# Kernel tuning notes

Hardware: AMD Instinct MI355X
Metric: run time of the kernel (lower is better)

The kernel has to match this reference:

```python
import jax, jax.numpy as jnp
import numpy as np

N_SRC_F = 40000; N_TGT_F = 40000; N_F = N_SRC_F + N_TGT_F
N_SRC_C = 1024; N_TGT_C = 1024; N_C = N_SRC_C + N_TGT_C
NN = 30        # KPConv neighbors per point
K = 15         # kernel points
C1 = 128       # fine-level feats (first_feats_dim)
C2 = 256       # coarse encoder out dim
GNN = 256      # gnn_feats_dim
HEADS = 4
DGCNN_K = 10
FINAL = 32     # final_feats_dim
EXT_F = 1.0; EXT_C = 2.0   # KPConv influence extents (scaled to unit-cube clouds)
EPS = 1e-12


def kpconv(q_pts, s_pts, s_feats, neighb, kpts, W, extent):
    # q_pts [Nq,3], s_pts [Ns,3], s_feats [Ns,Cin], neighb [Nq,NN], kpts [K,3], W [K,Cin,Cout]
    npts = s_pts[neighb]                              # [Nq,NN,3] irregular gather
    rel = npts - q_pts[:, None, :]
    # ||rel - kp||^2 expanded to avoid a [Nq,NN,K,3] intermediate
    d2 = (jnp.sum(rel * rel, -1)[:, :, None] + jnp.sum(kpts * kpts, -1)[None, None, :]
          - 2.0 * jnp.einsum('njd,kd->njk', rel, kpts))
    infl = jax.nn.relu(1.0 - jnp.sqrt(jnp.maximum(d2, EPS)) / extent)   # [Nq,NN,K]
    nf = s_feats[neighb]                              # [Nq,NN,Cin]
    h = jnp.einsum('njk,njc->nkc', infl, nf)          # kernel-point aggregation
    return jnp.einsum('nkc,kcd->nd', h, W)


def knn_idx(coords, k):
    sq = jnp.sum(coords * coords, -1)
    d2 = sq[:, None] + sq[None, :] - 2.0 * (coords @ coords.T)
    return jax.lax.top_k(-d2, k)[1]


def self_layer(coords, x, W, b):
    # DGCNN edge conv: knn on coords, edge = [x_i, x_j - x_i], 1x1 conv + relu, max over k
    idx = knn_idx(coords, DGCNN_K)
    neigh = x[idx]                                    # [N,k,C]
    ctr = jnp.broadcast_to(x[:, None, :], neigh.shape)
    edge = jnp.concatenate([ctr, neigh - ctr], -1)    # [N,k,2C]
    return jnp.max(jax.nn.relu(edge @ W + b), axis=1)


def cross_layer(x, y, Wq, Wk, Wv, Wm, bm):
    # multi-head cross attention x <- y, residual MLP on [x, message]
    N, C = x.shape
    dh = C // HEADS
    q = (x @ Wq).reshape(N, HEADS, dh)
    k = (y @ Wk).reshape(-1, HEADS, dh)
    v = (y @ Wv).reshape(-1, HEADS, dh)
    attn = jax.nn.softmax(jnp.einsum('nhd,mhd->hnm', q, k) / float(np.sqrt(dh)), axis=-1)
    msg = jnp.einsum('hnm,mhd->nhd', attn, v).reshape(N, C)
    return x + jnp.concatenate([x, msg], -1) @ Wm + bm


def l2norm(x):
    return x / jnp.maximum(jnp.linalg.norm(x, axis=1, keepdims=True), EPS)


def _forward(points_f, points_c, features, kernel_points_f, kernel_points_c,
             W_kp1, W_kp2, W_bottle, b_bottle, W_self1, b_self1,
             Wq, Wk, Wv, W_cross, b_cross, W_self2, b_self2,
             W_proj, b_proj, W_score, b_score, epsilon, W_dec, b_dec,
             neighbors_f, pool_idx, upsample_idx, len_src_c):
    # --- encoder: fine KPConv + strided KPConv to coarse ---
    x_f = kpconv(points_f, points_f, features, neighbors_f, kernel_points_f, W_kp1, EXT_F)  # [N_f,C1]
    skip = x_f
    x_c = kpconv(points_c, points_f, x_f, pool_idx, kernel_points_c, W_kp2, EXT_C)          # [N_c,C2]
    feats_c = x_c @ W_bottle + b_bottle                # bottleneck 1x1 conv -> [N_c,GNN]
    src, tgt = feats_c[:len_src_c], feats_c[len_src_c:]
    sc, tc = points_c[:len_src_c], points_c[len_src_c:]
    # --- GCN: self -> cross -> self (weights shared across src/tgt) ---
    src = self_layer(sc, src, W_self1, b_self1)
    tgt = self_layer(tc, tgt, W_self1, b_self1)
    src2 = cross_layer(src, tgt, Wq, Wk, Wv, W_cross, b_cross)
    tgt2 = cross_layer(tgt, src, Wq, Wk, Wv, W_cross, b_cross)
    src = self_layer(sc, src2, W_self2, b_self2)
    tgt = self_layer(tc, tgt2, W_self2, b_self2)
    feats = jnp.concatenate([src, tgt], 0) @ W_proj + b_proj   # proj_gnn
    scores_c_raw = feats @ W_score + b_score                   # proj_score [N_c,1]
    feats_norm = l2norm(feats)
    # --- bidirectional temperature-softmax matching head ---
    ip = feats_norm[:len_src_c] @ feats_norm[len_src_c:].T     # [Ns,Nt]
    temperature = jnp.exp(epsilon) + 0.03
    s1 = jax.nn.softmax(ip / temperature, axis=1) @ scores_c_raw[len_src_c:]
    s2 = jax.nn.softmax(ip.T / temperature, axis=1) @ scores_c_raw[:len_src_c]
    scores_saliency = jnp.concatenate([s1, s2], 0)
    # condition=True, add_cross_overlap=True branch
    x = jnp.concatenate([scores_c_raw, scores_saliency, feats], 1)    # [N_c, GNN+2]
    # --- decoder: nearest upsample + skip concat + unary conv ---
    x = jnp.concatenate([x[upsample_idx], skip], 1)            # [N_f, GNN+2+C1]
    x = x @ W_dec + b_dec                                      # [N_f, FINAL+2]
    feats_f = l2norm(x[:, :FINAL])
    so = jnp.clip(jax.nn.sigmoid(x[:, FINAL]), 0.0, 1.0)
    ss = jnp.clip(jax.nn.sigmoid(x[:, FINAL + 1]), 0.0, 1.0)
    so = jnp.where(jnp.isnan(so) | jnp.isinf(so), 0.0, so)     # regular_score
    ss = jnp.where(jnp.isnan(ss) | jnp.isinf(ss), 0.0, ss)
    return feats_f, so, ss


def _p(k, shape, fan):
    return jax.random.normal(k, shape, jnp.float32) / float(np.sqrt(fan))


def setup_inputs() -> dict:
    key = jax.random.key(0)
    ks = jax.random.split(key, 24)
    inp = {}
    inp['points_f'] = jax.random.uniform(ks[0], (N_F, 3), jnp.float32)
    inp['points_c'] = jax.random.uniform(ks[1], (N_C, 3), jnp.float32)
    inp['features'] = jnp.ones((N_F, 1), jnp.float32)
    inp['kernel_points_f'] = jax.random.normal(ks[2], (K, 3), jnp.float32) * 0.3
    inp['kernel_points_c'] = jax.random.normal(ks[3], (K, 3), jnp.float32) * 0.6
    inp['W_kp1'] = _p(ks[4], (K, 1, C1), K)
    inp['W_kp2'] = _p(ks[5], (K, C1, C2), K * C1)
    inp['W_bottle'] = _p(ks[6], (C2, GNN), C2); inp['b_bottle'] = jnp.zeros((GNN,), jnp.float32)
    inp['W_self1'] = _p(ks[7], (2 * GNN, GNN), 2 * GNN); inp['b_self1'] = jnp.zeros((GNN,), jnp.float32)
    inp['Wq'] = _p(ks[8], (GNN, GNN), GNN)
    inp['Wk'] = _p(ks[9], (GNN, GNN), GNN)
    inp['Wv'] = _p(ks[10], (GNN, GNN), GNN)
    inp['W_cross'] = _p(ks[11], (2 * GNN, GNN), 2 * GNN); inp['b_cross'] = jnp.zeros((GNN,), jnp.float32)
    inp['W_self2'] = _p(ks[12], (2 * GNN, GNN), 2 * GNN); inp['b_self2'] = jnp.zeros((GNN,), jnp.float32)
    inp['W_proj'] = _p(ks[13], (GNN, GNN), GNN); inp['b_proj'] = jnp.zeros((GNN,), jnp.float32)
    inp['W_score'] = _p(ks[14], (GNN, 1), GNN); inp['b_score'] = jnp.zeros((1,), jnp.float32)
    inp['epsilon'] = jnp.array(-5.0, jnp.float32)
    inp['W_dec'] = _p(ks[15], (GNN + 2 + C1, FINAL + 2), GNN + 2 + C1); inp['b_dec'] = jnp.zeros((FINAL + 2,), jnp.float32)
    inp['neighbors_f'] = jax.random.randint(ks[16], (N_F, NN), 0, N_F)
    inp['pool_idx'] = jax.random.randint(ks[17], (N_C, NN), 0, N_F)
    inp['upsample_idx'] = jax.random.randint(ks[18], (N_F,), 0, N_C)
    inp['len_src_c'] = N_SRC_C
    inp['len_src_f'] = N_SRC_F
    return inp


def reference(points_f, points_c, features, kernel_points_f, kernel_points_c,
              W_kp1, W_kp2, W_bottle, b_bottle, W_self1, b_self1,
              Wq, Wk, Wv, W_cross, b_cross, W_self2, b_self2,
              W_proj, b_proj, W_score, b_score, epsilon, W_dec, b_dec,
              neighbors_f, pool_idx, upsample_idx, len_src_c, len_src_f):
    return _forward(points_f, points_c, features, kernel_points_f, kernel_points_c,
                    W_kp1, W_kp2, W_bottle, b_bottle, W_self1, b_self1,
                    Wq, Wk, Wv, W_cross, b_cross, W_self2, b_self2,
                    W_proj, b_proj, W_score, b_score, epsilon, W_dec, b_dec,
                    neighbors_f, pool_idx, upsample_idx, len_src_c)
```

## Files before the change

### kernel.cpp

```cpp
#include <hip/hip_runtime.h>
#include <math.h>

#define NFINE   80000
#define NCRS    2048
#define NSRC    1024
#define NNB     30
#define KP      15
#define C1D     128
#define C2D     256
#define GD      256
#define DGK     10
#define FINALD  32
#define DECOUT  34

#define NCHUNK  8
#define CHUNK   128
#define TK      32
#define KC      4
#define KSTEP   480
#define GTR     16

__global__ __launch_bounds__(256) void kpconv_fine(
    const float* __restrict__ pts, const float* __restrict__ feat,
    const int* __restrict__ nbr, const float* __restrict__ kp,
    const float* __restrict__ W, float* __restrict__ out)
{
    int t = threadIdx.x, w = t >> 6, lane = t & 63;
    int n = blockIdx.x * 4 + w;
    __shared__ float contrib[4][NNB][17];
    __shared__ float h[4][KP + 1];
    float kx[KP], ky[KP], kz[KP], kk[KP];
#pragma unroll
    for (int k = 0; k < KP; k++) {
        kx[k] = kp[k*3]; ky[k] = kp[k*3+1]; kz[k] = kp[k*3+2];
        kk[k] = kx[k]*kx[k] + ky[k]*ky[k] + kz[k]*kz[k];
    }
    if (lane < NNB) {
        float qx = pts[n*3], qy = pts[n*3+1], qz = pts[n*3+2];
        int id = nbr[n*NNB + lane];
        float rx = pts[id*3]-qx, ry = pts[id*3+1]-qy, rz = pts[id*3+2]-qz;
        float rr = rx*rx + ry*ry + rz*rz;
        float f = feat[id];
#pragma unroll
        for (int k = 0; k < KP; k++) {
            float d2 = rr + kk[k] - 2.f*(rx*kx[k] + ry*ky[k] + rz*kz[k]);
            float infl = fmaxf(1.f - sqrtf(fmaxf(d2, 1e-12f)), 0.f);
            contrib[w][lane][k] = infl * f;
        }
    }
    __syncthreads();
// ... 65 lines not shown
    int t = threadIdx.x;
    int rg = blockIdx.x >> 2, kc = blockIdx.x & 3;
    int n0 = rg * GTR, kb0 = kc * KSTEP;
    __shared__ float xi[GTR][KSTEP];
    float* xf = &xi[0][0];
    for (int i = t; i < GTR*KSTEP; i += 256) {
        int r = i / KSTEP, c = i - r*KSTEP;
        xf[i] = hhg[(size_t)(n0 + r)*(KP*C1D) + kb0 + c];
    }
    __syncthreads();
    float a[GTR];
#pragma unroll
    for (int r = 0; r < GTR; r++) a[r] = 0.f;
    for (int c = 0; c < KSTEP; c += 4) {
        float w0 = W[(size_t)(kb0+c+0)*C2D + t];
        float w1 = W[(size_t)(kb0+c+1)*C2D + t];
        float w2 = W[(size_t)(kb0+c+2)*C2D + t];
        float w3 = W[(size_t)(kb0+c+3)*C2D + t];
#pragma unroll
        for (int r = 0; r < GTR; r++) {
            float4 xv = *(const float4*)&xi[r][c];
            a[r] += xv.x*w0 + xv.y*w1 + xv.z*w2 + xv.w*w3;
        }
    }
#pragma unroll
    for (int r = 0; r < GTR; r++)
        pbuf[(size_t)kc*NCRS*C2D + (size_t)(n0+r)*C2D + t] = a[r];
}

__global__ __launch_bounds__(256) void bottle_fused(
    const float* __restrict__ pbuf, const float* __restrict__ Wb,
    const float* __restrict__ b, float* __restrict__ out)
{
    int t = threadIdx.x, n0 = blockIdx.x * 8;
    const size_t MN = (size_t)NCRS*C2D;
    __shared__ float xi[8][C2D];
    for (int i = t; i < 8*C2D; i += 256) {
        int r = i >> 8, c = i & 255;
        size_t off = (size_t)(n0+r)*C2D + c;
        xi[r][c] = pbuf[off] + pbuf[MN+off] + pbuf[2*MN+off] + pbuf[3*MN+off];
    }
    __syncthreads();
    float a[8];
#pragma unroll
    for (int r = 0; r < 8; r++) a[r] = 0.f;
    for (int c = 0; c < C2D; c += 4) {
        float w0 = Wb[(c+0)*GD + t];
        float w1 = Wb[(c+1)*GD + t];
        float w2 = Wb[(c+2)*GD + t];
        float w3 = Wb[(c+3)*GD + t];
#pragma unroll
        for (int r = 0; r < 8; r++) {
            float4 xv = *(const float4*)&xi[r][c];
            a[r] += xv.x*w0 + xv.y*w1 + xv.z*w2 + xv.w*w3;
        }
    }
    float bv = b[t];
#pragma unroll
    for (int r = 0; r < 8; r++) out[(size_t)(n0+r)*GD + t] = a[r] + bv;
}

__global__ __launch_bounds__(512) void self_gemm(
    const float* __restrict__ x, const float* __restrict__ W,
    float* __restrict__ Y)
{
    int t = threadIdx.x, n0 = blockIdx.x * 8;
    __shared__ float xi[8][GD];
    for (int i = t; i < 8*GD; i += 512) {
        int r = i >> 8, c = i & 255;
        xi[r][c] = x[(size_t)(n0+r)*GD + c];
    }
    __syncthreads();
    const float* wcol = (t < GD) ? (W + t) : (W + (size_t)GD*GD + (t - GD));
    float a[8];
#pragma unroll
    for (int r = 0; r < 8; r++) a[r] = 0.f;
    for (int c = 0; c < GD; c += 4) {
        float w0 = wcol[(size_t)(c+0)*GD];
        float w1 = wcol[(size_t)(c+1)*GD];
        float w2 = wcol[(size_t)(c+2)*GD];
        float w3 = wcol[(size_t)(c+3)*GD];
#pragma unroll
        for (int r = 0; r < 8; r++) {
            float4 xv = *(const float4*)&xi[r][c];
            a[r] += xv.x*w0 + xv.y*w1 + xv.z*w2 + xv.w*w3;
        }
    }
#pragma unroll
    for (int r = 0; r < 8; r++) Y[(size_t)(n0+r)*512 + t] = a[r];
}

__global__ __launch_bounds__(256) void edge_max(
    const float* __restrict__ Y, const int* __restrict__ knn,
    const float* __restrict__ b, float* __restrict__ out)
{
    int n = blockIdx.x, t = threadIdx.x;
    int base = (n < NSRC) ? 0 : NSRC;
    __shared__ int ids[DGK];
    if (t < DGK) ids[t] = base + knn[n*DGK + t];
    __syncthreads();
    float a  = Y[(size_t)n*512 + t];
    float bn = Y[(size_t)n*512 + GD + t];
    float cst = a - bn + b[t];
    float acc = 0.f;
#pragma unroll
    for (int j = 0; j < DGK; j++) {
        float bj = Y[(size_t)ids[j]*512 + GD + t];
        acc = fmaxf(acc, fmaxf(cst + bj, 0.f));
    }
    out[(size_t)n*GD + t] = acc;
}

__global__ __launch_bounds__(256) void qkv_kernel(
    const float* __restrict__ x, const float* __restrict__ Wq,
    const float* __restrict__ Wk, const float* __restrict__ Wv,
    float* __restrict__ qb, float* __restrict__ kb, float* __restrict__ vb)
{
    int t = threadIdx.x, n0 = blockIdx.x * 8;
    __shared__ float xi[8][GD];
    for (int i = t; i < 8*GD; i += 256) {
        int r = i >> 8, c = i & 255;
        xi[r][c] = x[(size_t)(n0+r)*GD + c];
    }
    __syncthreads();
    const float* Ws[3] = {Wq, Wk, Wv};
    float* outs[3] = {qb, kb, vb};
#pragma unroll
    for (int m = 0; m < 3; m++) {
        const float* W = Ws[m];
        float a[8];
#pragma unroll
        for (int r = 0; r < 8; r++) a[r] = 0.f;
        for (int c = 0; c < GD; c += 4) {
            float w0 = W[(c+0)*GD + t];
            float w1 = W[(c+1)*GD + t];
            float w2 = W[(c+2)*GD + t];
            float w3 = W[(c+3)*GD + t];
#pragma unroll
            for (int r = 0; r < 8; r++) {
                float4 xv = *(const float4*)&xi[r][c];
                a[r] += xv.x*w0 + xv.y*w1 + xv.z*w2 + xv.w*w3;
            }
        }
        float* o = outs[m];
#pragma unroll
        for (int r = 0; r < 8; r++) o[(size_t)(n0+r)*GD + t] = a[r];
    }
}

__global__ __launch_bounds__(256) void knn_kernel(
    const float* __restrict__ pts, int* __restrict__ knn)
{
    int g = blockIdx.x;
    int t = threadIdx.x;
    int base = (g < NSRC) ? 0 : NSRC;
    int local = g - base;
    const float* P = pts + (size_t)base*3;
    __shared__ float d2s[NSRC];
    __shared__ float wval[4];
    __shared__ int   widx[4];
    float qx = P[local*3], qy = P[local*3+1], qz = P[local*3+2];
    float sqn = qx*qx + qy*qy + qz*qz;
#pragma unroll
    for (int ii = 0; ii < 4; ii++) {
        int m = t + ii*256;
        float px = P[m*3], py = P[m*3+1], pz = P[m*3+2];
        float sqm = px*px + py*py + pz*pz;
        d2s[m] = sqn + sqm - 2.f*(qx*px + qy*py + qz*pz);
    }
    __syncthreads();
    for (int r = 0; r < DGK; r++) {
        float bv = 3.4e38f; int bidx = NSRC;
#pragma unroll
        for (int ii = 0; ii < 4; ii++) {
            int m = t + ii*256;
            float v = d2s[m];
            if (v < bv) { bv = v; bidx = m; }
        }
#pragma unroll
// ... 19 lines not shown
}

__global__ __launch_bounds__(256) void attn_flash(
    const float* __restrict__ qb, const float* __restrict__ kb,
    const float* __restrict__ vb, float* __restrict__ pm,
    float* __restrict__ pl, float* __restrict__ pacc)
{
    int bidx = blockIdx.x;
    int h = bidx & 3, chunk = (bidx >> 2) & 7, rb = bidx >> 5;
    int t = threadIdx.x;
    int u = t >> 2, li = t & 3;
    int row0 = rb * 128 + u * 2;
    int kbase = (row0 < NSRC) ? NSRC : 0;

    __shared__ float4 kt[2][TK][16];
    __shared__ float4 vt[2][TK][16];

    const float4* kb4 = (const float4*)kb;
    const float4* vb4 = (const float4*)vb;
    size_t gbase = ((size_t)(kbase + chunk*CHUNK)) * 64 + h*16;

    float4 q0[4], q1[4];
    const float4* qa = (const float4*)(qb + (size_t)row0*GD + h*64 + li*16);
    const float4* qc = (const float4*)(qb + (size_t)(row0+1)*GD + h*64 + li*16);
#pragma unroll
    for (int i = 0; i < 4; i++) { q0[i] = qa[i]; q1[i] = qc[i]; }
    float4 a0[4], a1[4];
#pragma unroll
    for (int i = 0; i < 4; i++) {
        a0[i] = make_float4(0.f, 0.f, 0.f, 0.f);
        a1[i] = make_float4(0.f, 0.f, 0.f, 0.f);
    }
    float mr0 = -INFINITY, lr0 = 0.f, mr1 = -INFINITY, lr1 = 0.f;

    int f0 = t, f1 = t + 256;
    float4 rk0, rk1, rv0, rv1;

    {
        size_t tb = gbase;
        rk0 = kb4[tb + (size_t)(f0>>4)*64 + (f0&15)];
        rk1 = kb4[tb + (size_t)(f1>>4)*64 + (f1&15)];
        rv0 = vb4[tb + (size_t)(f0>>4)*64 + (f0&15)];
        rv1 = vb4[tb + (size_t)(f1>>4)*64 + (f1&15)];
        kt[0][f0>>4][f0&15] = rk0;  kt[0][f1>>4][f1&15] = rk1;
        vt[0][f0>>4][f0&15] = rv0;  vt[0][f1>>4][f1&15] = rv1;
    }
    __syncthreads();

    const int NT = CHUNK / TK;
    for (int tile = 0; tile < NT; tile++) {
        int cur = tile & 1;
        if (tile + 1 < NT) {
            size_t tb = gbase + (size_t)(tile+1)*TK*64;
            rk0 = kb4[tb + (size_t)(f0>>4)*64 + (f0&15)];
            rk1 = kb4[tb + (size_t)(f1>>4)*64 + (f1&15)];
            rv0 = vb4[tb + (size_t)(f0>>4)*64 + (f0&15)];
            rv1 = vb4[tb + (size_t)(f1>>4)*64 + (f1&15)];
        }
#pragma unroll 4
        for (int j = 0; j < TK; j++) {
            float4 k0 = kt[cur][j][li*4+0];
            float4 k1 = kt[cur][j][li*4+1];
            float4 k2 = kt[cur][j][li*4+2];
            float4 k3 = kt[cur][j][li*4+3];
            float pA = q0[0].x*k0.x + q0[0].y*k0.y + q0[0].z*k0.z + q0[0].w*k0.w
                     + q0[1].x*k1.x + q0[1].y*k1.y + q0[1].z*k1.z + q0[1].w*k1.w
                     + q0[2].x*k2.x + q0[2].y*k2.y + q0[2].z*k2.z + q0[2].w*k2.w
                     + q0[3].x*k3.x + q0[3].y*k3.y + q0[3].z*k3.z + q0[3].w*k3.w;
            float pB = q1[0].x*k0.x + q1[0].y*k0.y + q1[0].z*k0.z + q1[0].w*k0.w
                     + q1[1].x*k1.x + q1[1].y*k1.y + q1[1].z*k1.z + q1[1].w*k1.w
                     + q1[2].x*k2.x + q1[2].y*k2.y + q1[2].z*k2.z + q1[2].w*k2.w
                     + q1[3].x*k3.x + q1[3].y*k3.y + q1[3].z*k3.z + q1[3].w*k3.w;
            pA += __shfl_xor(pA, 1);  pB += __shfl_xor(pB, 1);
            pA += __shfl_xor(pA, 2);  pB += __shfl_xor(pB, 2);
            pA *= 0.125f;  pB *= 0.125f;
            float mn0 = fmaxf(mr0, pA);
            float mn1 = fmaxf(mr1, pB);
            float sc0 = __expf(mr0 - mn0), e0 = __expf(pA - mn0);
            float sc1 = __expf(mr1 - mn1), e1 = __expf(pB - mn1);
            lr0 = lr0*sc0 + e0;  lr1 = lr1*sc1 + e1;
            float4 v0 = vt[cur][j][li*4+0];
            float4 v1 = vt[cur][j][li*4+1];
            float4 v2 = vt[cur][j][li*4+2];
            float4 v3 = vt[cur][j][li*4+3];
            a0[0].x = a0[0].x*sc0 + e0*v0.x; a0[0].y = a0[0].y*sc0 + e0*v0.y;
            a0[0].z = a0[0].z*sc0 + e0*v0.z; a0[0].w = a0[0].w*sc0 + e0*v0.w;
            a0[1].x = a0[1].x*sc0 + e0*v1.x; a0[1].y = a0[1].y*sc0 + e0*v1.y;
            a0[1].z = a0[1].z*sc0 + e0*v1.z; a0[1].w = a0[1].w*sc0 + e0*v1.w;
            a0[2].x = a0[2].x*sc0 + e0*v2.x; a0[2].y = a0[2].y*sc0 + e0*v2.y;
            a0[2].z = a0[2].z*sc0 + e0*v2.z; a0[2].w = a0[2].w*sc0 + e0*v2.w;
            a0[3].x = a0[3].x*sc0 + e0*v3.x; a0[3].y = a0[3].y*sc0 + e0*v3.y;
            a0[3].z = a0[3].z*sc0 + e0*v3.z; a0[3].w = a0[3].w*sc0 + e0*v3.w;
            a1[0].x = a1[0].x*sc1 + e1*v0.x; a1[0].y = a1[0].y*sc1 + e1*v0.y;
            a1[0].z = a1[0].z*sc1 + e1*v0.z; a1[0].w = a1[0].w*sc1 + e1*v0.w;
            a1[1].x = a1[1].x*sc1 + e1*v1.x; a1[1].y = a1[1].y*sc1 + e1*v1.y;
            a1[1].z = a1[1].z*sc1 + e1*v1.z; a1[1].w = a1[1].w*sc1 + e1*v1.w;
            a1[2].x = a1[2].x*sc1 + e1*v2.x; a1[2].y = a1[2].y*sc1 + e1*v2.y;
            a1[2].z = a1[2].z*sc1 + e1*v2.z; a1[2].w = a1[2].w*sc1 + e1*v2.w;
            a1[3].x = a1[3].x*sc1 + e1*v3.x; a1[3].y = a1[3].y*sc1 + e1*v3.y;
            a1[3].z = a1[3].z*sc1 + e1*v3.z; a1[3].w = a1[3].w*sc1 + e1*v3.w;
            mr0 = mn0;  mr1 = mn1;
        }
        if (tile + 1 < NT) {
            __syncthreads();
            int nb = (tile + 1) & 1;
            kt[nb][f0>>4][f0&15] = rk0;  kt[nb][f1>>4][f1&15] = rk1;
            vt[nb][f0>>4][f0&15] = rv0;  vt[nb][f1>>4][f1&15] = rv1;
            __syncthreads();
        }
    }
    int pi0 = (chunk*4 + h)*NCRS + row0;
    if (li == 0) { pm[pi0] = mr0; pl[pi0] = lr0; pm[pi0+1] = mr1; pl[pi0+1] = lr1; }
    float4* po0 = (float4*)(pacc + (size_t)pi0*64);
    float4* po1 = (float4*)(pacc + (size_t)(pi0+1)*64);
#pragma unroll
    for (int i = 0; i < 4; i++) { po0[li*4 + i] = a0[i]; po1[li*4 + i] = a1[i]; }
}

__global__ __launch_bounds__(256) void attn_combine(
    const float* __restrict__ pm, const float* __restrict__ pl,
    const float* __restrict__ pacc, float* __restrict__ msg)
{
    int row = blockIdx.x, t = threadIdx.x;
    int h = t >> 6, d = t & 63;
    float m = -INFINITY;
#pragma unroll
    for (int c = 0; c < NCHUNK; c++) m = fmaxf(m, pm[(c*4 + h)*NCRS + row]);
    float lsum = 0.f, asum = 0.f;
#pragma unroll
    for (int c = 0; c < NCHUNK; c++) {
        int pi = (c*4 + h)*NCRS + row;
        float w = __expf(pm[pi] - m);
        lsum += pl[pi] * w;
        asum += pacc[(size_t)pi*64 + d] * w;
    }
    msg[(size_t)row*GD + h*64 + d] = asum / lsum;
}

__global__ __launch_bounds__(256) void cross_combine(
    const float* __restrict__ x, const float* __restrict__ msg,
    const float* __restrict__ Wm, const float* __restrict__ bm,
    float* __restrict__ out)
{
    int t = threadIdx.x, n0 = blockIdx.x * 8;
    __shared__ float xs[8][GD], ms[8][GD];
    for (int i = t; i < 8*GD; i += 256) {
        int r = i >> 8, c = i & 255;
        xs[r][c] = x[(size_t)(n0+r)*GD + c];
        ms[r][c] = msg[(size_t)(n0+r)*GD + c];
    }
    __syncthreads();
    float bv = bm[t];
    float a[8];
#pragma unroll
    for (int r = 0; r < 8; r++) a[r] = bv;
    for (int c = 0; c < GD; c += 4) {
        float w10 = Wm[(c+0)*GD + t];
        float w11 = Wm[(c+1)*GD + t];
        float w12 = Wm[(c+2)*GD + t];
        float w13 = Wm[(c+3)*GD + t];
        float w20 = Wm[(GD+c+0)*GD + t];
        float w21 = Wm[(GD+c+1)*GD + t];
        float w22 = Wm[(GD+c+2)*GD + t];
        float w23 = Wm[(GD+c+3)*GD + t];
#pragma unroll
        for (int r = 0; r < 8; r++) {
            float4 xv = *(const float4*)&xs[r][c];
            float4 mv = *(const float4*)&ms[r][c];
            a[r] += xv.x*w10 + xv.y*w11 + xv.z*w12 + xv.w*w13
                  + mv.x*w20 + mv.y*w21 + mv.z*w22 + mv.w*w23;
        }
    }
#pragma unroll
    for (int r = 0; r < 8; r++)
        out[(size_t)(n0+r)*GD + t] = xs[r][t] + a[r];
}

__global__ __launch_bounds__(256) void proj_gemm(
    const float* __restrict__ x, const float* __restrict__ W,
    const float* __restrict__ b, float* __restrict__ out)
{
    int t = threadIdx.x, n0 = blockIdx.x * 8;
    __shared__ float xi[8][GD];
    for (int i = t; i < 8*GD; i += 256) {
        int r = i >> 8, c = i & 255;
        xi[r][c] = x[(size_t)(n0+r)*GD + c];
    }
    __syncthreads();
    float a[8];
#pragma unroll
    for (int r = 0; r < 8; r++) a[r] = 0.f;
    for (int c = 0; c < GD; c += 4) {
        float w0 = W[(c+0)*GD + t];
        float w1 = W[(c+1)*GD + t];
        float w2 = W[(c+2)*GD + t];
        float w3 = W[(c+3)*GD + t];
#pragma unroll
        for (int r = 0; r < 8; r++) {
            float4 xv = *(const float4*)&xi[r][c];
            a[r] += xv.x*w0 + xv.y*w1 + xv.z*w2 + xv.w*w3;
        }
    }
    float bv = b[t];
#pragma unroll
    for (int r = 0; r < 8; r++) out[(size_t)(n0+r)*GD + t] = a[r] + bv;
}

__global__ __launch_bounds__(256) void norm_score(
    const float* __restrict__ feats, const float* __restrict__ Wsc,
    const float* __restrict__ bsc, float* __restrict__ fnorm,
    float* __restrict__ scores)
{
    int t = threadIdx.x, lane = t & 63, w = t >> 6;
    int n0 = blockIdx.x * 8;
#pragma unroll
    for (int rr = 0; rr < 2; rr++) {
        int r = n0 + w*2 + rr;
        float q0 = feats[(size_t)r*GD + lane];
        float q1 = feats[(size_t)r*GD + 64 + lane];
        float q2 = feats[(size_t)r*GD + 128 + lane];
        float q3 = feats[(size_t)r*GD + 192 + lane];
        float sq = q0*q0 + q1*q1 + q2*q2 + q3*q3;
        float sc = q0*Wsc[lane] + q1*Wsc[64+lane] + q2*Wsc[128+lane] + q3*Wsc[192+lane];
#pragma unroll
        for (int off = 32; off >= 1; off >>= 1) {
            sq += __shfl_xor(sq, off);
            sc += __shfl_xor(sc, off);
        }
        float inv = 1.f / fmaxf(sqrtf(sq), 1e-12f);
        fnorm[(size_t)r*GD + lane]       = q0*inv;
        fnorm[(size_t)r*GD + 64 + lane]  = q1*inv;
        fnorm[(size_t)r*GD + 128 + lane] = q2*inv;
        fnorm[(size_t)r*GD + 192 + lane] = q3*inv;
        if (lane == 0) scores[r] = sc + bsc[0];
    }
}

__global__ __launch_bounds__(256) void ip_kernel(
    const float* __restrict__ fnorm, float* __restrict__ ip)
{
    int t = threadIdx.x;
    int n0 = (blockIdx.x >> 2) * 4;
    int m  = (blockIdx.x & 3) * 256 + t;
    __shared__ float xs[GD][4];
    for (int i = t; i < 4*GD; i += 256) {
        int r = i >> 8, c = i & 255;
        xs[c][r] = fnorm[(size_t)(n0+r)*GD + c];
    }
    __syncthreads();
    const float4* fr = (const float4*)(fnorm + (size_t)(NSRC + m)*GD);
    float a0 = 0.f, a1 = 0.f, a2 = 0.f, a3 = 0.f;
    for (int c4 = 0; c4 < GD/4; c4++) {
        float4 f = fr[c4];
        float4 xa = *(const float4*)&xs[c4*4+0][0];
        float4 xb = *(const float4*)&xs[c4*4+1][0];
        float4 xc = *(const float4*)&xs[c4*4+2][0];
        float4 xd = *(const float4*)&xs[c4*4+3][0];
        a0 += f.x*xa.x + f.y*xb.x + f.z*xc.x + f.w*xd.x;
        a1 += f.x*xa.y + f.y*xb.y + f.z*xc.y + f.w*xd.y;
        a2 += f.x*xa.z + f.y*xb.z + f.z*xc.z + f.w*xd.z;
        a3 += f.x*xa.w + f.y*xb.w + f.z*xc.w + f.w*xd.w;
    }
    ip[(size_t)(n0+0)*NSRC + m] = a0;
    ip[(size_t)(n0+1)*NSRC + m] = a1;
    ip[(size_t)(n0+2)*NSRC + m] = a2;
    ip[(size_t)(n0+3)*NSRC + m] = a3;
}

template<bool COL>
__global__ __launch_bounds__(256) void saliency_kernel(
    const float* __restrict__ ip, const float* __restrict__ scores_other,
    const float* __restrict__ epsv, float* __restrict__ sal_out)
{
    int n = blockIdx.x, t = threadIdx.x;
    float T = expf(epsv[0]) + 0.03f;
    __shared__ float red[256];
    float vals[4];
    float m = -INFINITY;
#pragma unroll
    for (int ii = 0; ii < 4; ii++) {
        int i = t + ii*256;
        float vv = COL ? ip[(size_t)i*NSRC + n] : ip[(size_t)n*NSRC + i];
        vv /= T;
        vals[ii] = vv;
        m = fmaxf(m, vv);
    }
    red[t] = m; __syncthreads();
    for (int s = 128; s > 0; s >>= 1) { if (t < s) red[t] = fmaxf(red[t], red[t+s]); __syncthreads(); }
    float mx = red[0]; __syncthreads();
    float se = 0.f, wsum = 0.f;
#pragma unroll
    for (int ii = 0; ii < 4; ii++) {
        int i = t + ii*256;
        float e = expf(vals[ii] - mx);
        se += e; wsum += e * scores_other[i];
    }
    red[t] = se; __syncthreads();
    for (int s = 128; s > 0; s >>= 1) { if (t < s) red[t] += red[t+s]; __syncthreads(); }
    float S = red[0]; __syncthreads();
    red[t] = wsum; __syncthreads();
    for (int s = 128; s > 0; s >>= 1) { if (t < s) red[t] += red[t+s]; __syncthreads(); }
    if (t == 0) sal_out[n] = red[0] / S;
}

__global__ __launch_bounds__(256) void dec_coarse(
    const float* __restrict__ scores, const float* __restrict__ sal,
    const float* __restrict__ feats, const float* __restrict__ Wd,
    const float* __restrict__ bd, float* __restrict__ decfeat)
{
    int t = threadIdx.x, lane = t & 63, w = t >> 6;
    int n = blockIdx.x * 4 + w;
    __shared__ float xr[4][GD];
    for (int c = lane; c < GD; c += 64) xr[w][c] = feats[(size_t)n*GD + c];
    float acc = 0.f;
    if (lane < DECOUT) {
        acc = bd[lane] + scores[n]*Wd[lane] + sal[n]*Wd[DECOUT + lane];
        for (int c = 0; c < GD; c++) acc += xr[w][c] * Wd[(2 + c)*DECOUT + lane];
    }
    if (lane < 40) decfeat[(size_t)n*40 + lane] = (lane < DECOUT) ? acc : 0.f;
}

__global__ __launch_bounds__(256) void decoder_kernel(
    const float* __restrict__ decfeat, const float* __restrict__ skip,
    const int* __restrict__ ups, const float* __restrict__ Wd,
    float* __restrict__ outf, float* __restrict__ outso,
    float* __restrict__ outss)
{
    int t = threadIdx.x;
    __shared__ float wsk[C1D*36];
    for (int i = t; i < C1D*36; i += 256) {
        int cc = i / 36, j = i - cc*36;
        wsk[i] = (j < DECOUT) ? Wd[(size_t)(2 + GD + cc)*DECOUT + j] : 0.f;
    }
    __syncthreads();
    int row = blockIdx.x * 256 + t;
// ... 46 lines not shown
    const float* kp_c         = (const float*)d_in[4];
    const float* W_kp1        = (const float*)d_in[5];
    const float* W_kp2        = (const float*)d_in[6];
    const float* W_bottle     = (const float*)d_in[7];
    const float* b_bottle     = (const float*)d_in[8];
    const float* W_self1      = (const float*)d_in[9];
    const float* b_self1      = (const float*)d_in[10];
    const float* Wq           = (const float*)d_in[11];
    const float* Wk           = (const float*)d_in[12];
    const float* Wv           = (const float*)d_in[13];
    const float* W_cross      = (const float*)d_in[14];
    const float* b_cross      = (const float*)d_in[15];
    const float* W_self2      = (const float*)d_in[16];
    const float* b_self2      = (const float*)d_in[17];
    const float* W_proj       = (const float*)d_in[18];
    const float* b_proj       = (const float*)d_in[19];
    const float* W_score      = (const float*)d_in[20];
    const float* b_score      = (const float*)d_in[21];
    const float* epsilon      = (const float*)d_in[22];
    const float* W_dec        = (const float*)d_in[23];
    const float* b_dec        = (const float*)d_in[24];
    const int*   neighbors_f  = (const int*)d_in[25];
    const int*   pool_idx     = (const int*)d_in[26];
    const int*   upsample_idx = (const int*)d_in[27];

    float* ws = (float*)d_ws;
    size_t o = 0;
    auto alloc = [&](size_t nfl) { float* p = ws + o; o += (nfl + 63) & ~(size_t)63; return p; };
    float* x_f     = alloc((size_t)NFINE * C1D);
    float* g1      = alloc((size_t)NCRS * GD);
    float* qb      = alloc((size_t)NCRS * GD);
    float* kb      = alloc((size_t)NCRS * GD);
    float* vb      = alloc((size_t)NCRS * GD);
    float* msg     = alloc((size_t)NCRS * GD);
    float* feats_c = alloc((size_t)NCRS * GD);
    float* scores  = alloc(NCRS);
    float* sal     = alloc(NCRS);
    float* decfeat = alloc((size_t)NCRS * 40);
    int*   knn_b   = (int*)alloc(NCRS * DGK);

    const size_t NG = (size_t)NCRS * GD;
    const size_t MN = (size_t)NCRS * C2D;
    size_t usz = 4*MN + (size_t)NCRS*KP*C1D;
    float* U = alloc(usz);
    float* pbuf = U;
    float* hhg  = U + 4*MN;
    float* Y1   = U;
    float* pm   = U;
    float* pl   = U + (size_t)NCRS*4*NCHUNK;
    float* pacc = U + (size_t)2*NCRS*4*NCHUNK;
    float* g2   = U;
    float* Y2   = U + NG;
    float* g3   = U + 3*NG;
    float* feats= U + 4*NG;
    float* fnorm= U + 5*NG;
    float* ip   = U + 6*NG;

    float* outf  = (float*)d_out;
    float* outso = outf + (size_t)NFINE * FINALD;
    float* outss = outso + NFINE;

    kpconv_fine<<<NFINE/4, 256, 0, stream>>>(points_f, features, neighbors_f, kp_f, W_kp1, x_f);
    hh_kernel<<<NCRS, 256, 0, stream>>>(points_c, points_f, x_f, pool_idx, kp_c, hhg);
    hh_gemm<<<(NCRS/GTR)*KC, 256, 0, stream>>>(hhg, W_kp2, pbuf);
    bottle_fused<<<NCRS/8, 256, 0, stream>>>(pbuf, W_bottle, b_bottle, feats_c);

    knn_kernel<<<NCRS, 256, 0, stream>>>(points_c, knn_b);
    self_gemm<<<NCRS/8, 512, 0, stream>>>(feats_c, W_self1, Y1);
    edge_max<<<NCRS, 256, 0, stream>>>(Y1, knn_b, b_self1, g1);
    qkv_kernel<<<NCRS/8, 256, 0, stream>>>(g1, Wq, Wk, Wv, qb, kb, vb);
    attn_flash<<<512, 256, 0, stream>>>(qb, kb, vb, pm, pl, pacc);
    attn_combine<<<NCRS, 256, 0, stream>>>(pm, pl, pacc, msg);
    cross_combine<<<NCRS/8, 256, 0, stream>>>(g1, msg, W_cross, b_cross, g2);
    self_gemm<<<NCRS/8, 512, 0, stream>>>(g2, W_self2, Y2);
    edge_max<<<NCRS, 256, 0, stream>>>(Y2, knn_b, b_self2, g3);

    proj_gemm<<<NCRS/8, 256, 0, stream>>>(g3, W_proj, b_proj, feats);
    norm_score<<<NCRS/8, 256, 0, stream>>>(feats, W_score, b_score, fnorm, scores);
    ip_kernel<<<NSRC, 256, 0, stream>>>(fnorm, ip);
    saliency_kernel<false><<<NSRC, 256, 0, stream>>>(ip, scores + NSRC, epsilon, sal);
    saliency_kernel<true><<<NSRC, 256, 0, stream>>>(ip, scores, epsilon, sal + NSRC);

    dec_coarse<<<NCRS/4, 256, 0, stream>>>(scores, sal, feats, W_dec, b_dec, decfeat);
    decoder_kernel<<<(NFINE + 255)/256, 256, 0, stream>>>(decfeat, x_f, upsample_idx,
                                                          W_dec, outf, outso, outss);
}
```

Measured before the change: 499.9 us.

## Fuse attention combine, proj+norm, saliency kernels; halve GEMM row tiles; batch softmax

The attention combine step is folded into the cross-attention MLP kernel, and the projection GEMM is fused with L2-normalisation and scoring. The two saliency launches become one. Coarse GEMM kernels process 4 rows per block instead of 8, doubling block count for more parallelism on the 2048-row problems. The flash-attention inner loop now takes a per-tile max and rescales once per tile, with TK reduced to 16; this trades per-key rescale work for register arrays holding the scores.

```diff
diff --git a/kernel.cpp b/kernel.cpp
--- a/kernel.cpp
+++ b/kernel.cpp
@@ -15,7 +15,7 @@
 
 #define NCHUNK  8
 #define CHUNK   128
-#define TK      32
+#define TK      16
 #define KC      4
 #define KSTEP   480
 #define GTR     16
@@ -147,62 +147,62 @@
     const float* __restrict__ pbuf, const float* __restrict__ Wb,
     const float* __restrict__ b, float* __restrict__ out)
 {
-    int t = threadIdx.x, n0 = blockIdx.x * 8;
+    int t = threadIdx.x, n0 = blockIdx.x * 4;
     const size_t MN = (size_t)NCRS*C2D;
-    __shared__ float xi[8][C2D];
-    for (int i = t; i < 8*C2D; i += 256) {
+    __shared__ float xi[4][C2D];
+    for (int i = t; i < 4*C2D; i += 256) {
         int r = i >> 8, c = i & 255;
         size_t off = (size_t)(n0+r)*C2D + c;
         xi[r][c] = pbuf[off] + pbuf[MN+off] + pbuf[2*MN+off] + pbuf[3*MN+off];
     }
     __syncthreads();
-    float a[8];
-#pragma unroll
-    for (int r = 0; r < 8; r++) a[r] = 0.f;
+    float a[4];
+#pragma unroll
+    for (int r = 0; r < 4; r++) a[r] = 0.f;
     for (int c = 0; c < C2D; c += 4) {
         float w0 = Wb[(c+0)*GD + t];
         float w1 = Wb[(c+1)*GD + t];
         float w2 = Wb[(c+2)*GD + t];
         float w3 = Wb[(c+3)*GD + t];
 #pragma unroll
-        for (int r = 0; r < 8; r++) {
+        for (int r = 0; r < 4; r++) {
             float4 xv = *(const float4*)&xi[r][c];
             a[r] += xv.x*w0 + xv.y*w1 + xv.z*w2 + xv.w*w3;
         }
     }
     float bv = b[t];
 #pragma unroll
-    for (int r = 0; r < 8; r++) out[(size_t)(n0+r)*GD + t] = a[r] + bv;
+    for (int r = 0; r < 4; r++) out[(size_t)(n0+r)*GD + t] = a[r] + bv;
 }
 
 __global__ __launch_bounds__(512) void self_gemm(
     const float* __restrict__ x, const float* __restrict__ W,
     float* __restrict__ Y)
 {
-    int t = threadIdx.x, n0 = blockIdx.x * 8;
-    __shared__ float xi[8][GD];
-    for (int i = t; i < 8*GD; i += 512) {
+    int t = threadIdx.x, n0 = blockIdx.x * 4;
+    __shared__ float xi[4][GD];
+    for (int i = t; i < 4*GD; i += 512) {
         int r = i >> 8, c = i & 255;
         xi[r][c] = x[(size_t)(n0+r)*GD + c];
     }
     __syncthreads();
     const float* wcol = (t < GD) ? (W + t) : (W + (size_t)GD*GD + (t - GD));
-    float a[8];
-#pragma unroll
-    for (int r = 0; r < 8; r++) a[r] = 0.f;
+    float a[4];
+#pragma unroll
+    for (int r = 0; r < 4; r++) a[r] = 0.f;
     for (int c = 0; c < GD; c += 4) {
         float w0 = wcol[(size_t)(c+0)*GD];
         float w1 = wcol[(size_t)(c+1)*GD];
         float w2 = wcol[(size_t)(c+2)*GD];
         float w3 = wcol[(size_t)(c+3)*GD];
 #pragma unroll
-        for (int r = 0; r < 8; r++) {
+        for (int r = 0; r < 4; r++) {
             float4 xv = *(const float4*)&xi[r][c];
             a[r] += xv.x*w0 + xv.y*w1 + xv.z*w2 + xv.w*w3;
         }
     }
 #pragma unroll
-    for (int r = 0; r < 8; r++) Y[(size_t)(n0+r)*512 + t] = a[r];
+    for (int r = 0; r < 4; r++) Y[(size_t)(n0+r)*512 + t] = a[r];
 }
 
 __global__ __launch_bounds__(256) void edge_max(
@@ -231,9 +231,9 @@
     const float* __restrict__ Wk, const float* __restrict__ Wv,
     float* __restrict__ qb, float* __restrict__ kb, float* __restrict__ vb)
 {
-    int t = threadIdx.x, n0 = blockIdx.x * 8;
-    __shared__ float xi[8][GD];
-    for (int i = t; i < 8*GD; i += 256) {
+    int t = threadIdx.x, n0 = blockIdx.x * 4;
+    __shared__ float xi[4][GD];
+    for (int i = t; i < 4*GD; i += 256) {
         int r = i >> 8, c = i & 255;
         xi[r][c] = x[(size_t)(n0+r)*GD + c];
     }
@@ -243,23 +243,23 @@
 #pragma unroll
     for (int m = 0; m < 3; m++) {
         const float* W = Ws[m];
-        float a[8];
-#pragma unroll
-        for (int r = 0; r < 8; r++) a[r] = 0.f;
+        float a[4];
+#pragma unroll
+        for (int r = 0; r < 4; r++) a[r] = 0.f;
         for (int c = 0; c < GD; c += 4) {
             float w0 = W[(c+0)*GD + t];
             float w1 = W[(c+1)*GD + t];
             float w2 = W[(c+2)*GD + t];
             float w3 = W[(c+3)*GD + t];
 #pragma unroll
-            for (int r = 0; r < 8; r++) {
+            for (int r = 0; r < 4; r++) {
                 float4 xv = *(const float4*)&xi[r][c];
                 a[r] += xv.x*w0 + xv.y*w1 + xv.z*w2 + xv.w*w3;
             }
         }
         float* o = outs[m];
 #pragma unroll
-        for (int r = 0; r < 8; r++) o[(size_t)(n0+r)*GD + t] = a[r];
+        for (int r = 0; r < 4; r++) o[(size_t)(n0+r)*GD + t] = a[r];
     }
 }
 
@@ -345,18 +345,16 @@
         a1[i] = make_float4(0.f, 0.f, 0.f, 0.f);
     }
     float mr0 = -INFINITY, lr0 = 0.f, mr1 = -INFINITY, lr1 = 0.f;
-
-    int f0 = t, f1 = t + 256;
-    float4 rk0, rk1, rv0, rv1;
-
+    float p0[TK], p1[TK];
+
+    int f = t;
+    float4 rk, rv;
     {
         size_t tb = gbase;
-        rk0 = kb4[tb + (size_t)(f0>>4)*64 + (f0&15)];
-        rk1 = kb4[tb + (size_t)(f1>>4)*64 + (f1&15)];
-        rv0 = vb4[tb + (size_t)(f0>>4)*64 + (f0&15)];
-        rv1 = vb4[tb + (size_t)(f1>>4)*64 + (f1&15)];
-        kt[0][f0>>4][f0&15] = rk0;  kt[0][f1>>4][f1&15] = rk1;
-        vt[0][f0>>4][f0&15] = rv0;  vt[0][f1>>4][f1&15] = rv1;
+        rk = kb4[tb + (size_t)(f>>4)*64 + (f&15)];
+        rv = vb4[tb + (size_t)(f>>4)*64 + (f&15)];
+        kt[0][f>>4][f&15] = rk;
+        vt[0][f>>4][f&15] = rv;
     }
     __syncthreads();
 
@@ -365,12 +363,11 @@
         int cur = tile & 1;
         if (tile + 1 < NT) {
             size_t tb = gbase + (size_t)(tile+1)*TK*64;
-            rk0 = kb4[tb + (size_t)(f0>>4)*64 + (f0&15)];
-            rk1 = kb4[tb + (size_t)(f1>>4)*64 + (f1&15)];
-            rv0 = vb4[tb + (size_t)(f0>>4)*64 + (f0&15)];
-            rv1 = vb4[tb + (size_t)(f1>>4)*64 + (f1&15)];
-        }
-#pragma unroll 4
+            rk = kb4[tb + (size_t)(f>>4)*64 + (f&15)];
+            rv = vb4[tb + (size_t)(f>>4)*64 + (f&15)];
+        }
+        float tm0 = -INFINITY, tm1 = -INFINITY;
+#pragma unroll
         for (int j = 0; j < TK; j++) {
             float4 k0 = kt[cur][j][li*4+0];
             float4 k1 = kt[cur][j][li*4+1];
@@ -387,38 +384,41 @@
             pA += __shfl_xor(pA, 1);  pB += __shfl_xor(pB, 1);
             pA += __shfl_xor(pA, 2);  pB += __shfl_xor(pB, 2);
             pA *= 0.125f;  pB *= 0.125f;
-            float mn0 = fmaxf(mr0, pA);
-            float mn1 = fmaxf(mr1, pB);
-            float sc0 = __expf(mr0 - mn0), e0 = __expf(pA - mn0);
-            float sc1 = __expf(mr1 - mn1), e1 = __expf(pB - mn1);
-            lr0 = lr0*sc0 + e0;  lr1 = lr1*sc1 + e1;
+            p0[j] = pA;  p1[j] = pB;
+            tm0 = fmaxf(tm0, pA);  tm1 = fmaxf(tm1, pB);
+        }
+        float mn0 = fmaxf(mr0, tm0), mn1 = fmaxf(mr1, tm1);
+        float sc0 = __expf(mr0 - mn0), sc1 = __expf(mr1 - mn1);
+        lr0 *= sc0;  lr1 *= sc1;
+#pragma unroll
+        for (int i = 0; i < 4; i++) {
+            a0[i].x *= sc0; a0[i].y *= sc0; a0[i].z *= sc0; a0[i].w *= sc0;
+            a1[i].x *= sc1; a1[i].y *= sc1; a1[i].z *= sc1; a1[i].w *= sc1;
+        }
+        mr0 = mn0;  mr1 = mn1;
+#pragma unroll
+        for (int j = 0; j < TK; j++) {
+            float e0 = __expf(p0[j] - mn0);
+            float e1 = __expf(p1[j] - mn1);
+            lr0 += e0;  lr1 += e1;
             float4 v0 = vt[cur][j][li*4+0];
             float4 v1 = vt[cur][j][li*4+1];
             float4 v2 = vt[cur][j][li*4+2];
             float4 v3 = vt[cur][j][li*4+3];
-            a0[0].x = a0[0].x*sc0 + e0*v0.x; a0[0].y = a0[0].y*sc0 + e0*v0.y;
-            a0[0].z = a0[0].z*sc0 + e0*v0.z; a0[0].w = a0[0].w*sc0 + e0*v0.w;
-            a0[1].x = a0[1].x*sc0 + e0*v1.x; a0[1].y = a0[1].y*sc0 + e0*v1.y;
-            a0[1].z = a0[1].z*sc0 + e0*v1.z; a0[1].w = a0[1].w*sc0 + e0*v1.w;
-            a0[2].x = a0[2].x*sc0 + e0*v2.x; a0[2].y = a0[2].y*sc0 + e0*v2.y;
-            a0[2].z = a0[2].z*sc0 + e0*v2.z; a0[2].w = a0[2].w*sc0 + e0*v2.w;
-            a0[3].x = a0[3].x*sc0 + e0*v3.x; a0[3].y = a0[3].y*sc0 + e0*v3.y;
-            a0[3].z = a0[3].z*sc0 + e0*v3.z; a0[3].w = a0[3].w*sc0 + e0*v3.w;
-            a1[0].x = a1[0].x*sc1 + e1*v0.x; a1[0].y = a1[0].y*sc1 + e1*v0.y;
-            a1[0].z = a1[0].z*sc1 + e1*v0.z; a1[0].w = a1[0].w*sc1 + e1*v0.w;
-            a1[1].x = a1[1].x*sc1 + e1*v1.x; a1[1].y = a1[1].y*sc1 + e1*v1.y;
-            a1[1].z = a1[1].z*sc1 + e1*v1.z; a1[1].w = a1[1].w*sc1 + e1*v1.w;
-            a1[2].x = a1[2].x*sc1 + e1*v2.x; a1[2].y = a1[2].y*sc1 + e1*v2.y;
-            a1[2].z = a1[2].z*sc1 + e1*v2.z; a1[2].w = a1[2].w*sc1 + e1*v2.w;
-            a1[3].x = a1[3].x*sc1 + e1*v3.x; a1[3].y = a1[3].y*sc1 + e1*v3.y;
-            a1[3].z = a1[3].z*sc1 + e1*v3.z; a1[3].w = a1[3].w*sc1 + e1*v3.w;
-            mr0 = mn0;  mr1 = mn1;
+            a0[0].x += e0*v0.x; a0[0].y += e0*v0.y; a0[0].z += e0*v0.z; a0[0].w += e0*v0.w;
+            a0[1].x += e0*v1.x; a0[1].y += e0*v1.y; a0[1].z += e0*v1.z; a0[1].w += e0*v1.w;
+            a0[2].x += e0*v2.x; a0[2].y += e0*v2.y; a0[2].z += e0*v2.z; a0[2].w += e0*v2.w;
+            a0[3].x += e0*v3.x; a0[3].y += e0*v3.y; a0[3].z += e0*v3.z; a0[3].w += e0*v3.w;
+            a1[0].x += e1*v0.x; a1[0].y += e1*v0.y; a1[0].z += e1*v0.z; a1[0].w += e1*v0.w;
+            a1[1].x += e1*v1.x; a1[1].y += e1*v1.y; a1[1].z += e1*v1.z; a1[1].w += e1*v1.w;
+            a1[2].x += e1*v2.x; a1[2].y += e1*v2.y; a1[2].z += e1*v2.z; a1[2].w += e1*v2.w;
+            a1[3].x += e1*v3.x; a1[3].y += e1*v3.y; a1[3].z += e1*v3.z; a1[3].w += e1*v3.w;
         }
         if (tile + 1 < NT) {
             __syncthreads();
             int nb = (tile + 1) & 1;
-            kt[nb][f0>>4][f0&15] = rk0;  kt[nb][f1>>4][f1&15] = rk1;
-            vt[nb][f0>>4][f0&15] = rv0;  vt[nb][f1>>4][f1&15] = rv1;
+            kt[nb][f>>4][f&15] = rk;
+            vt[nb][f>>4][f&15] = rv;
             __syncthreads();
         }
     }
@@ -430,43 +430,38 @@
     for (int i = 0; i < 4; i++) { po0[li*4 + i] = a0[i]; po1[li*4 + i] = a1[i]; }
 }
 
-__global__ __launch_bounds__(256) void attn_combine(
-    const float* __restrict__ pm, const float* __restrict__ pl,
-    const float* __restrict__ pacc, float* __restrict__ msg)
-{
-    int row = blockIdx.x, t = threadIdx.x;
-    int h = t >> 6, d = t & 63;
-    float m = -INFINITY;
-#pragma unroll
-    for (int c = 0; c < NCHUNK; c++) m = fmaxf(m, pm[(c*4 + h)*NCRS + row]);
-    float lsum = 0.f, asum = 0.f;
-#pragma unroll
-    for (int c = 0; c < NCHUNK; c++) {
-        int pi = (c*4 + h)*NCRS + row;
-        float w = __expf(pm[pi] - m);
-        lsum += pl[pi] * w;
-        asum += pacc[(size_t)pi*64 + d] * w;
-    }
-    msg[(size_t)row*GD + h*64 + d] = asum / lsum;
-}
-
-__global__ __launch_bounds__(256) void cross_combine(
-    const float* __restrict__ x, const float* __restrict__ msg,
+__global__ __launch_bounds__(256) void cross_fused(
+    const float* __restrict__ x, const float* __restrict__ pm,
+    const float* __restrict__ pl, const float* __restrict__ pacc,
     const float* __restrict__ Wm, const float* __restrict__ bm,
     float* __restrict__ out)
 {
-    int t = threadIdx.x, n0 = blockIdx.x * 8;
-    __shared__ float xs[8][GD], ms[8][GD];
-    for (int i = t; i < 8*GD; i += 256) {
+    int t = threadIdx.x, n0 = blockIdx.x * 4;
+    int h = t >> 6, d = t & 63;
+    __shared__ float xs[4][GD], ms[4][GD];
+    for (int i = t; i < 4*GD; i += 256) {
         int r = i >> 8, c = i & 255;
         xs[r][c] = x[(size_t)(n0+r)*GD + c];
-        ms[r][c] = msg[(size_t)(n0+r)*GD + c];
+    }
+#pragma unroll
+    for (int r = 0; r < 4; r++) {
+        int row = n0 + r;
+        float m = -INFINITY;
+#pragma unroll
+        for (int c = 0; c < NCHUNK; c++) m = fmaxf(m, pm[(c*4 + h)*NCRS + row]);
+        float lsum = 0.f, asum = 0.f;
+#pragma unroll
+        for (int c = 0; c < NCHUNK; c++) {
+            int pi = (c*4 + h)*NCRS + row;
+            float w = __expf(pm[pi] - m);
+            lsum += pl[pi] * w;
+            asum += pacc[(size_t)pi*64 + d] * w;
+        }
+        ms[r][t] = asum / lsum;
     }
     __syncthreads();
     float bv = bm[t];
-    float a[8];
-#pragma unroll
-    for (int r = 0; r < 8; r++) a[r] = bv;
+    float a[4] = {bv, bv, bv, bv};
     for (int c = 0; c < GD; c += 4) {
         float w10 = Wm[(c+0)*GD + t];
         float w11 = Wm[(c+1)*GD + t];
@@ -477,7 +472,7 @@
         float w22 = Wm[(GD+c+2)*GD + t];
         float w23 = Wm[(GD+c+3)*GD + t];
 #pragma unroll
-        for (int r = 0; r < 8; r++) {
+        for (int r = 0; r < 4; r++) {
             float4 xv = *(const float4*)&xs[r][c];
             float4 mv = *(const float4*)&ms[r][c];
             a[r] += xv.x*w10 + xv.y*w11 + xv.z*w12 + xv.w*w13
@@ -485,68 +480,60 @@
         }
     }
 #pragma unroll
-    for (int r = 0; r < 8; r++)
+    for (int r = 0; r < 4; r++)
         out[(size_t)(n0+r)*GD + t] = xs[r][t] + a[r];
 }
 
-__global__ __launch_bounds__(256) void proj_gemm(
+__global__ __launch_bounds__(256) void proj_norm(
     const float* __restrict__ x, const float* __restrict__ W,
-    const float* __restrict__ b, float* __restrict__ out)
-{
-    int t = threadIdx.x, n0 = blockIdx.x * 8;
-    __shared__ float xi[8][GD];
-    for (int i = t; i < 8*GD; i += 256) {
+    const float* __restrict__ b, const float* __restrict__ Wsc,
+    const float* __restrict__ bsc, float* __restrict__ feats,
+    float* __restrict__ fnorm, float* __restrict__ scores)
+{
+    int t = threadIdx.x, n0 = blockIdx.x * 4;
+    __shared__ float xi[4][GD];
+    __shared__ float pf[4][GD];
+    for (int i = t; i < 4*GD; i += 256) {
         int r = i >> 8, c = i & 255;
         xi[r][c] = x[(size_t)(n0+r)*GD + c];
     }
     __syncthreads();
-    float a[8];
-#pragma unroll
-    for (int r = 0; r < 8; r++) a[r] = 0.f;
+    float a[4] = {0.f, 0.f, 0.f, 0.f};
     for (int c = 0; c < GD; c += 4) {
         float w0 = W[(c+0)*GD + t];
         float w1 = W[(c+1)*GD + t];
         float w2 = W[(c+2)*GD + t];
         float w3 = W[(c+3)*GD + t];
 #pragma unroll
-        for (int r = 0; r < 8; r++) {
+        for (int r = 0; r < 4; r++) {
             float4 xv = *(const float4*)&xi[r][c];
             a[r] += xv.x*w0 + xv.y*w1 + xv.z*w2 + xv.w*w3;
         }
     }
     float bv = b[t];
 #pragma unroll
-    for (int r = 0; r < 8; r++) out[(size_t)(n0+r)*GD + t] = a[r] + bv;
-}
-
-__global__ __launch_bounds__(256) void norm_score(
-    const float* __restrict__ feats, const float* __restrict__ Wsc,
-    const float* __restrict__ bsc, float* __restrict__ fnorm,
-    float* __restrict__ scores)
-{
-    int t = threadIdx.x, lane = t & 63, w = t >> 6;
-    int n0 = blockIdx.x * 8;
-#pragma unroll
-    for (int rr = 0; rr < 2; rr++) {
-        int r = n0 + w*2 + rr;
-        float q0 = feats[(size_t)r*GD + lane];
-        float q1 = feats[(size_t)r*GD + 64 + lane];
-        float q2 = feats[(size_t)r*GD + 128 + lane];
-        float q3 = feats[(size_t)r*GD + 192 + lane];
-        float sq = q0*q0 + q1*q1 + q2*q2 + q3*q3;
-        float sc = q0*Wsc[lane] + q1*Wsc[64+lane] + q2*Wsc[128+lane] + q3*Wsc[192+lane];
-#pragma unroll
-        for (int off = 32; off >= 1; off >>= 1) {
-            sq += __shfl_xor(sq, off);
-            sc += __shfl_xor(sc, off);
-        }
-        float inv = 1.f / fmaxf(sqrtf(sq), 1e-12f);
-        fnorm[(size_t)r*GD + lane]       = q0*inv;
-        fnorm[(size_t)r*GD + 64 + lane]  = q1*inv;
-        fnorm[(size_t)r*GD + 128 + lane] = q2*inv;
-        fnorm[(size_t)r*GD + 192 + lane] = q3*inv;
-        if (lane == 0) scores[r] = sc + bsc[0];
-    }
+    for (int r = 0; r < 4; r++) {
+        float v = a[r] + bv;
+        feats[(size_t)(n0+r)*GD + t] = v;
+        pf[r][t] = v;
+    }
+    __syncthreads();
+    int lane = t & 63, w = t >> 6;
+    int rr = n0 + w;
+    float q0 = pf[w][lane], q1 = pf[w][64+lane], q2 = pf[w][128+lane], q3 = pf[w][192+lane];
+    float sq = q0*q0 + q1*q1 + q2*q2 + q3*q3;
+    float sc = q0*Wsc[lane] + q1*Wsc[64+lane] + q2*Wsc[128+lane] + q3*Wsc[192+lane];
+#pragma unroll
+    for (int off = 32; off >= 1; off >>= 1) {
+        sq += __shfl_xor(sq, off);
+        sc += __shfl_xor(sc, off);
+    }
+    float inv = 1.f / fmaxf(sqrtf(sq), 1e-12f);
+    fnorm[(size_t)rr*GD + lane]       = q0*inv;
+    fnorm[(size_t)rr*GD + 64 + lane]  = q1*inv;
+    fnorm[(size_t)rr*GD + 128 + lane] = q2*inv;
+    fnorm[(size_t)rr*GD + 192 + lane] = q3*inv;
+    if (lane == 0) scores[rr] = sc + bsc[0];
 }
 
 __global__ __launch_bounds__(256) void ip_kernel(
@@ -580,12 +567,14 @@
     ip[(size_t)(n0+3)*NSRC + m] = a3;
 }
 
-template<bool COL>
-__global__ __launch_bounds__(256) void saliency_kernel(
-    const float* __restrict__ ip, const float* __restrict__ scores_other,
+__global__ __launch_bounds__(256) void saliency_all(
+    const float* __restrict__ ip, const float* __restrict__ scores,
     const float* __restrict__ epsv, float* __restrict__ sal_out)
 {
-    int n = blockIdx.x, t = threadIdx.x;
+    int g = blockIdx.x, t = threadIdx.x;
+    bool col = (g >= NSRC);
+    int n = col ? (g - NSRC) : g;
+    const float* so = col ? scores : (scores + NSRC);
     float T = expf(epsv[0]) + 0.03f;
     __shared__ float red[256];
     float vals[4];
@@ -593,7 +582,7 @@
 #pragma unroll
     for (int ii = 0; ii < 4; ii++) {
         int i = t + ii*256;
-        float vv = COL ? ip[(size_t)i*NSRC + n] : ip[(size_t)n*NSRC + i];
+        float vv = col ? ip[(size_t)i*NSRC + n] : ip[(size_t)n*NSRC + i];
         vv /= T;
         vals[ii] = vv;
         m = fmaxf(m, vv);
@@ -606,14 +595,14 @@
     for (int ii = 0; ii < 4; ii++) {
         int i = t + ii*256;
         float e = expf(vals[ii] - mx);
-        se += e; wsum += e * scores_other[i];
+        se += e; wsum += e * so[i];
     }
     red[t] = se; __syncthreads();
     for (int s = 128; s > 0; s >>= 1) { if (t < s) red[t] += red[t+s]; __syncthreads(); }
     float S = red[0]; __syncthreads();
     red[t] = wsum; __syncthreads();
     for (int s = 128; s > 0; s >>= 1) { if (t < s) red[t] += red[t+s]; __syncthreads(); }
-    if (t == 0) sal_out[n] = red[0] / S;
+    if (t == 0) sal_out[g] = red[0] / S;
 }
 
 __global__ __launch_bounds__(256) void dec_coarse(
@@ -726,7 +715,6 @@
     float* qb      = alloc((size_t)NCRS * GD);
     float* kb      = alloc((size_t)NCRS * GD);
     float* vb      = alloc((size_t)NCRS * GD);
-    float* msg     = alloc((size_t)NCRS * GD);
     float* feats_c = alloc((size_t)NCRS * GD);
     float* scores  = alloc(NCRS);
     float* sal     = alloc(NCRS);
@@ -735,21 +723,22 @@
 
     const size_t NG = (size_t)NCRS * GD;
     const size_t MN = (size_t)NCRS * C2D;
+    const size_t PMN = (size_t)NCRS * 4 * NCHUNK;
     size_t usz = 4*MN + (size_t)NCRS*KP*C1D;
     float* U = alloc(usz);
     float* pbuf = U;
     float* hhg  = U + 4*MN;
     float* Y1   = U;
     float* pm   = U;
-    float* pl   = U + (size_t)NCRS*4*NCHUNK;
-    float* pacc = U + (size_t)2*NCRS*4*NCHUNK;
-    float* g2   = U;
-    float* Y2   = U + NG;
-    float* g3   = U + 3*NG;
-    float* feats= U + 4*NG;
-    float* fnorm= U + 5*NG;
-    float* ip   = U + 6*NG;
-
+    float* pl   = U + PMN;
+    float* pacc = U + 2*PMN;
+    float* g2   = U + 2*PMN + PMN*64;
+    float* Y2   = U;
+    float* g3   = U + 2*NG;
+    float* feats= U + 3*NG;
+    float* fnorm= U + 4*NG;
+    float* ip   = U + 5*NG;
+    
     float* outf  = (float*)d_out;
     float* outso = outf + (size_t)NFINE * FINALD;
     float* outss = outso + NFINE;
@@ -757,23 +746,21 @@
     kpconv_fine<<<NFINE/4, 256, 0, stream>>>(points_f, features, neighbors_f, kp_f, W_kp1, x_f);
     hh_kernel<<<NCRS, 256, 0, stream>>>(points_c, points_f, x_f, pool_idx, kp_c, hhg);
     hh_gemm<<<(NCRS/GTR)*KC, 256, 0, stream>>>(hhg, W_kp2, pbuf);
-    bottle_fused<<<NCRS/8, 256, 0, stream>>>(pbuf, W_bottle, b_bottle, feats_c);
+    bottle_fused<<<NCRS/4, 256, 0, stream>>>(pbuf, W_bottle, b_bottle, feats_c);
 
     knn_kernel<<<NCRS, 256, 0, stream>>>(points_c, knn_b);
-    self_gemm<<<NCRS/8, 512, 0, stream>>>(feats_c, W_self1, Y1);
+    self_gemm<<<NCRS/4, 512, 0, stream>>>(feats_c, W_self1, Y1);
     edge_max<<<NCRS, 256, 0, stream>>>(Y1, knn_b, b_self1, g1);
-    qkv_kernel<<<NCRS/8, 256, 0, stream>>>(g1, Wq, Wk, Wv, qb, kb, vb);
+    qkv_kernel<<<NCRS/4, 256, 0, stream>>>(g1, Wq, Wk, Wv, qb, kb, vb);
     attn_flash<<<512, 256, 0, stream>>>(qb, kb, vb, pm, pl, pacc);
-    attn_combine<<<NCRS, 256, 0, stream>>>(pm, pl, pacc, msg);
-    cross_combine<<<NCRS/8, 256, 0, stream>>>(g1, msg, W_cross, b_cross, g2);
-    self_gemm<<<NCRS/8, 512, 0, stream>>>(g2, W_self2, Y2);
+    cross_fused<<<NCRS/4, 256, 0, stream>>>(g1, pm, pl, pacc, W_cross, b_cross, g2);
+    self_gemm<<<NCRS/4, 512, 0, stream>>>(g2, W_self2, Y2);
     edge_max<<<NCRS, 256, 0, stream>>>(Y2, knn_b, b_self2, g3);
 
-    proj_gemm<<<NCRS/8, 256, 0, stream>>>(g3, W_proj, b_proj, feats);
-    norm_score<<<NCRS/8, 256, 0, stream>>>(feats, W_score, b_score, fnorm, scores);
+    proj_norm<<<NCRS/4, 256, 0, stream>>>(g3, W_proj, b_proj, W_score, b_score,
+                                          feats, fnorm, scores);
     ip_kernel<<<NSRC, 256, 0, stream>>>(fnorm, ip);
-    saliency_kernel<false><<<NSRC, 256, 0, stream>>>(ip, scores + NSRC, epsilon, sal);
-    saliency_kernel<true><<<NSRC, 256, 0, stream>>>(ip, scores, epsilon, sal + NSRC);
+    saliency_all<<<NCRS, 256, 0, stream>>>(ip, scores, epsilon, sal);
 
     dec_coarse<<<NCRS/4, 256, 0, stream>>>(scores, sal, feats, W_dec, b_dec, decfeat);
     decoder_kernel<<<(NFINE + 255)/256, 256, 0, stream>>>(decfeat, x_f, upsample_idx,
```

Result: faster. 470.7 us (-5.8%).
